# Kernel optimization log

Hardware: AMD Instinct MI355X
Metric: run time of the kernel (lower is better)

The kernel has to match this reference:

```python
import jax, jax.numpy as jnp
import numpy as np

DIM = 256
L = 16            # block_size (query rows per leaf block)
H = 8             # num_heads
D = DIM // H      # head_dim = 32
KC = L + 1        # key count: L leaf nodes + 1 block (mean) node, layout '16x17'
B = 2
N = 32768         # multiple of L -> no padding path
NB = N // L       # 2048 blocks
SCALE = D ** -0.5


def setup_inputs() -> dict:
    key = jax.random.key(0)
    ks = jax.random.split(key, 8)
    x = jax.random.normal(ks[0], (B, N, DIM), jnp.float32)
    attn_mask = jax.random.randint(ks[1], (NB, L, KC), 0, 2, dtype=jnp.int32)
    ar = jnp.arange(L)
    attn_mask = attn_mask.at[:, ar, ar].set(1)  # self always visible -> no all-masked rows
    edge_feats = jax.random.normal(ks[2], (NB, L, KC, 4), jnp.float32)
    s = DIM ** -0.5
    Wqkv = jax.random.normal(ks[3], (3 * DIM, DIM), jnp.float32) * s
    bqkv = jnp.zeros((3 * DIM,), jnp.float32)
    Wproj = jax.random.normal(ks[4], (DIM, DIM), jnp.float32) * s
    bproj = jnp.zeros((DIM,), jnp.float32)
    Wgate = jax.random.normal(ks[5], (H, 4), jnp.float32) * 0.01  # nn.init.normal_(std=0.01)
    bgate = jnp.zeros((H,), jnp.float32)
    return {"x": x, "attn_mask": attn_mask, "edge_feats": edge_feats,
            "Wqkv": Wqkv, "bqkv": bqkv, "Wproj": Wproj, "bproj": bproj,
            "Wgate": Wgate, "bgate": bgate}


def reference(x, attn_mask, edge_feats, Wqkv, bqkv, Wproj, bproj, Wgate, bgate):
    # x: [B, N, C] -> blocks [B, NB, L, C]
    x_blk = x.reshape(B, NB, L, DIM)
    block_node = x_blk.mean(axis=2, keepdims=True)           # virtual block node
    kv = jnp.concatenate([x_blk, block_node], axis=2)         # [B, NB, KC, C]

    # qkv projections (slice of the fused Linear; rows are independent so math is identical)
    q = x_blk @ Wqkv[:DIM].T + bqkv[:DIM]
    k = kv @ Wqkv[DIM:2 * DIM].T + bqkv[DIM:2 * DIM]
    v = kv @ Wqkv[2 * DIM:].T + bqkv[2 * DIM:]
    q = q.reshape(B, NB, L, H, D)
    k = k.reshape(B, NB, KC, H, D)
    v = v.reshape(B, NB, KC, H, D)

    scores = jnp.einsum('bnqhd,bnkhd->bnqkh', q, k) * SCALE   # [B, NB, L, KC, H]

    # physics bias: zero out + set channel 3 = 1 for block node column and self (diagonal)
    ar = jnp.arange(L)
    unit = jnp.array([0.0, 0.0, 0.0, 1.0], edge_feats.dtype)
    bias = edge_feats.at[:, :, L, :].set(unit)                # block-node column
    bias = bias.at[:, ar, ar, :].set(unit)                    # self bias on diagonal
    bias = jnp.broadcast_to(bias[None], (B, NB, L, KC, 4))    # expand over batch

    scores = scores + bias[..., 3:4]

    mask0 = (attn_mask[None] == 0)[..., None]                 # [1, NB, L, KC, 1]
    scores = jnp.where(mask0, -jnp.inf, scores)
    attn = jax.nn.softmax(scores, axis=3)

    gate = jnp.einsum('bnqkf,hf->bnqkh', bias, Wgate) + bgate  # edge-conditioned gate
    gate = jnp.where(mask0, 0.0, gate)

    combined = attn + gate
    out = jnp.einsum('bnqkh,bnkhd->bnqhd', combined, v).reshape(B, N, DIM)
    return out @ Wproj.T + bproj
```

## Files before the change

### kernel.cpp

```cpp
#include <hip/hip_runtime.h>
#include <cstdint>
#include <cstddef>

#define B_SZ 2
#define N_SEQ 32768
#define NB 2048
#define HD 32
#define LQ 16
#define KCNT 17
#define M_ROWS 65536
#define SCALE_F 0.17677669529663687f

typedef __attribute__((ext_vector_type(8))) short sv8;
typedef __attribute__((ext_vector_type(4))) short sv4;
typedef __attribute__((ext_vector_type(4))) float f4;

__device__ __forceinline__ short f2bf(float f) {
  unsigned u = __builtin_bit_cast(unsigned, f);
  u = (u + 0x7FFFu + ((u >> 16) & 1u)) >> 16;
  return (short)u;
}
__device__ __forceinline__ float bf2f(short s) {
  unsigned u = ((unsigned)(unsigned short)s) << 16;
  return __builtin_bit_cast(float, u);
}
__device__ __forceinline__ void gload16(const void* g, void* l) {
  __builtin_amdgcn_global_load_lds(
      (const __attribute__((address_space(1))) unsigned int*)g,
      (__attribute__((address_space(3))) unsigned int*)l, 16, 0, 0);
}
__device__ __forceinline__ f4 mfma16(sv8 a, sv8 b, f4 c) {
  return __builtin_amdgcn_mfma_f32_16x16x32_bf16(a, b, c, 0, 0, 0);
}

__global__ __launch_bounds__(256) void split256(const float* __restrict__ src,
                                                short* __restrict__ dst, int n4) {
  int i = blockIdx.x * 256 + threadIdx.x;
  if (i >= n4) return;
  float4 v = ((const float4*)src)[i];
  size_t row = (size_t)(i >> 6);
  int c = (i & 63) * 4;
  float fv[4] = {v.x, v.y, v.z, v.w};
  sv4 hi, lo;
#pragma unroll
  for (int j = 0; j < 4; ++j) {
    short h = f2bf(fv[j]);
    hi[j] = h;
    lo[j] = f2bf(fv[j] - bf2f(h));
  }
  *(sv4*)&dst[row * 512 + c] = hi;
  *(sv4*)&dst[row * 512 + 256 + c] = lo;
}

__global__ __launch_bounds__(256) void cast256(const float* __restrict__ src,
                                               short* __restrict__ dst, int n4) {
  int i = blockIdx.x * 256 + threadIdx.x;
  if (i >= n4) return;
  float4 v = ((const float4*)src)[i];
  sv4 h = {f2bf(v.x), f2bf(v.y), f2bf(v.z), f2bf(v.w)};
  *(sv4*)&dst[(size_t)i * 4] = h;
}

__global__ __launch_bounds__(256) void gemm_bf_qkv(
    const short* __restrict__ A1, const short* __restrict__ B2,
    const float* __restrict__ bias, short* __restrict__ Qbf,
    short* __restrict__ Kbf, short* __restrict__ Vbf) {
  __shared__ __align__(16) short Ahs[2][128][32];
  __shared__ __align__(16) short Bhs[2][128][32];
  const int tid = threadIdx.x;
  const int w = tid >> 6, l = tid & 63;
  const int wm = w >> 1, wn = w & 1;
  const int bid = blockIdx.x;
  const int chunk = (6 * 512) >> 3;
  const int lbid = (bid & 7) * chunk + (bid >> 3);
  const int nti = lbid % 6, mti = lbid / 6;
  const int m0 = mti * 128, n0 = nti * 128;
  const int lr = l >> 2;
  const int lc = (l & 3) * 8;
  const int fr = l & 15, kg = (l >> 4) * 8;
  f4 acc[4][4] = {};
#pragma unroll
  for (int i = 0; i < 2; ++i) {
    const int row = w * 32 + i * 16;
    gload16(A1 + (size_t)(m0 + row + lr) * 256 + lc, (void*)&Ahs[0][row][0]);
    gload16(B2 + (size_t)(n0 + row + lr) * 512 + lc, (void*)&Bhs[0][row][0]);
  }
  asm volatile("s_waitcnt vmcnt(0)" ::: "memory");
  __builtin_amdgcn_s_barrier();
  int cur = 0;
  for (int s = 0; s < 8; ++s) {
    if (s < 7) {
      const int sk = (s + 1) * 32;
#pragma unroll
      for (int i = 0; i < 2; ++i) {
        const int row = w * 32 + i * 16;
        gload16(A1 + (size_t)(m0 + row + lr) * 256 + sk + lc,
                (void*)&Ahs[cur ^ 1][row][0]);
        gload16(B2 + (size_t)(n0 + row + lr) * 512 + sk + lc,
                (void*)&Bhs[cur ^ 1][row][0]);
      }
    }
    if (s > 0) {
      if (s < 7) asm volatile("s_waitcnt vmcnt(4)" ::: "memory");
      else asm volatile("s_waitcnt vmcnt(0)" ::: "memory");
      __builtin_amdgcn_s_barrier();
    }
    sv8 fa[4], fb[4];
#pragma unroll
    for (int t = 0; t < 4; ++t) {
      fa[t] = *(const sv8*)&Ahs[cur][wm * 64 + t * 16 + fr][kg];
      fb[t] = *(const sv8*)&Bhs[cur][wn * 64 + t * 16 + fr][kg];
    }
#pragma unroll
    for (int mt = 0; mt < 4; ++mt)
#pragma unroll
      for (int nt = 0; nt < 4; ++nt)
        acc[mt][nt] = mfma16(fa[mt], fb[nt], acc[mt][nt]);
    asm volatile("s_waitcnt lgkmcnt(0)" ::: "memory");
    __builtin_amdgcn_s_barrier();
    cur ^= 1;
  }
  short* dst = (nti < 2) ? Qbf : ((nti < 4) ? Kbf : Vbf);
  const int r0 = (l >> 4) * 4;
#pragma unroll
  for (int mt = 0; mt < 4; ++mt)
#pragma unroll
    for (int nt = 0; nt < 4; ++nt) {
      const int n = n0 + wn * 64 + nt * 16 + fr;
      const float bv = bias[n];
      const int nn = n & 255;
      const size_t mb = (size_t)(m0 + wm * 64 + mt * 16 + r0);
#pragma unroll
      for (int j = 0; j < 4; ++j)
        dst[(mb + j) * 256 + nn] = f2bf(acc[mt][nt][j] + bv);
    }
}

__global__ __launch_bounds__(256) void gemm_proj1(
    const short* __restrict__ A1, const short* __restrict__ B2,
    const float* __restrict__ bias, float* __restrict__ C) {
  __shared__ __align__(16) short Ahs[2][128][32];
  __shared__ __align__(16) short Bhs[2][128][32];
  const int tid = threadIdx.x;
  const int w = tid >> 6, l = tid & 63;
  const int wm = w >> 1, wn = w & 1;
  const int bid = blockIdx.x;
  const int chunk = (2 * 512) >> 3;
  const int lbid = (bid & 7) * chunk + (bid >> 3);
  const int nti = lbid % 2, mti = lbid / 2;
  const int m0 = mti * 128, n0 = nti * 128;
  const int lr = l >> 2;
  const int lc = (l & 3) * 8;
  const int fr = l & 15, kg = (l >> 4) * 8;
  f4 acc[4][4] = {};
#pragma unroll
  for (int i = 0; i < 2; ++i) {
    const int row = w * 32 + i * 16;
    gload16(A1 + (size_t)(m0 + row + lr) * 256 + lc, (void*)&Ahs[0][row][0]);
    gload16(B2 + (size_t)(n0 + row + lr) * 512 + lc, (void*)&Bhs[0][row][0]);
  }
  asm volatile("s_waitcnt vmcnt(0)" ::: "memory");
  __builtin_amdgcn_s_barrier();
  int cur = 0;
  for (int s = 0; s < 8; ++s) {
    if (s < 7) {
      const int sk = (s + 1) * 32;
#pragma unroll
      for (int i = 0; i < 2; ++i) {
        const int row = w * 32 + i * 16;
        gload16(A1 + (size_t)(m0 + row + lr) * 256 + sk + lc,
                (void*)&Ahs[cur ^ 1][row][0]);
        gload16(B2 + (size_t)(n0 + row + lr) * 512 + sk + lc,
                (void*)&Bhs[cur ^ 1][row][0]);
      }
    }
    if (s > 0) {
      if (s < 7) asm volatile("s_waitcnt vmcnt(4)" ::: "memory");
      else asm volatile("s_waitcnt vmcnt(0)" ::: "memory");
      __builtin_amdgcn_s_barrier();
    }
    sv8 fa[4], fb[4];
#pragma unroll
    for (int t = 0; t < 4; ++t) {
      fa[t] = *(const sv8*)&Ahs[cur][wm * 64 + t * 16 + fr][kg];
      fb[t] = *(const sv8*)&Bhs[cur][wn * 64 + t * 16 + fr][kg];
    }
#pragma unroll
    for (int mt = 0; mt < 4; ++mt)
#pragma unroll
      for (int nt = 0; nt < 4; ++nt)
        acc[mt][nt] = mfma16(fa[mt], fb[nt], acc[mt][nt]);
    asm volatile("s_waitcnt lgkmcnt(0)" ::: "memory");
    __builtin_amdgcn_s_barrier();
    cur ^= 1;
  }
  const int r0 = (l >> 4) * 4;
#pragma unroll
  for (int mt = 0; mt < 4; ++mt)
#pragma unroll
    for (int nt = 0; nt < 4; ++nt) {
      const int n = n0 + wn * 64 + nt * 16 + fr;
      const float bv = bias[n];
      const size_t mb = (size_t)(m0 + wm * 64 + mt * 16 + r0);
#pragma unroll
      for (int j = 0; j < 4; ++j) C[(mb + j) * 256 + n] = acc[mt][nt][j] + bv;
    }
}

__global__ __launch_bounds__(256, 4) void attn_v7(
    const short* __restrict__ Qb, const short* __restrict__ Kb,
    const short* __restrict__ Vb, const int* __restrict__ amask,
    const float* __restrict__ efeat, const float* __restrict__ Wgate,
    const float* __restrict__ bgate, short* __restrict__ AO) {
  __shared__ __align__(16) short Kl[16 * 264];
  __shared__ __align__(16) short Vl[32 * 264];
  __shared__ __align__(16) short Ol[16 * 264];
  __shared__ float4 Es[LQ * KCNT];
  __shared__ int Ms[LQ * KCNT];

  const int tid = threadIdx.x, g = blockIdx.x;
  const int b = g >> 11, nb = g & (NB - 1);
  const size_t tok0 = (size_t)(b * N_SEQ + nb * LQ);
  const int w = tid >> 6, l = tid & 63;
  const int ln = l & 15, lg = l >> 4;
  const f4 fzero = {0.f, 0.f, 0.f, 0.f};

  sv8 qf[2];
#pragma unroll
  for (int hh = 0; hh < 2; ++hh) {
    const int h = w * 2 + hh;
    qf[hh] = *(const sv8*)(Qb + (tok0 + ln) * 256 + h * 32 + lg * 8);
  }

#pragma unroll
  for (int i = 0; i < 2; ++i) {
    const int f = tid + i * 256;
    const int t = f >> 5, c8 = (f & 31) * 8;
    *(sv8*)&Kl[t * 264 + c8] = *(const sv8*)(Kb + (tok0 + t) * 256 + c8);
    *(sv8*)&Vl[t * 264 + c8] = *(const sv8*)(Vb + (tok0 + t) * 256 + c8);
  }
  {
    const sv8 z = {};
    for (int z8 = tid; z8 < 528; z8 += 256) *(sv8*)&Vl[4224 + z8 * 8] = z;
  }
  {
    const float4* esrc = (const float4*)(efeat + (size_t)nb * LQ * KCNT * 4);
    const int* msrc = amask + (size_t)nb * LQ * KCNT;
    Es[tid] = esrc[tid];
    Ms[tid] = msrc[tid];
    if (tid < LQ * KCNT - 256) {
      Es[256 + tid] = esrc[256 + tid];
      Ms[256 + tid] = msrc[256 + tid];
    }
  }
  __syncthreads();

  const int q = ln;
#pragma unroll
  for (int hh = 0; hh < 2; ++hh) {
    const int h = w * 2 + hh;
    sv8 ka = *(const sv8*)&Kl[ln * 264 + h * 32 + lg * 8];
    f4 sr = mfma16(ka, qf[hh], fzero);

    const float wg0 = Wgate[h * 4], wg1 = Wgate[h * 4 + 1];
    const float wg2 = Wgate[h * 4 + 2], wg3 = Wgate[h * 4 + 3];
    const float bg = bgate[h];

    float rs = sr[0] + sr[1] + sr[2] + sr[3];
    rs += __shfl_xor(rs, 16);
    rs += __shfl_xor(rs, 32);

    float s_[4], gt_[4];
    int vis_[4];
#pragma unroll
    for (int j = 0; j < 4; ++j) {
      const int kc = lg * 4 + j;
      float e0, e1, e2, e3;
      if (kc == q) { e0 = e1 = e2 = 0.f; e3 = 1.f; }
      else { float4 e = Es[q * KCNT + kc]; e0 = e.x; e1 = e.y; e2 = e.z; e3 = e.w; }
      const int m = Ms[q * KCNT + kc];
      vis_[j] = m;
      s_[j] = sr[j] * SCALE_F + e3;
      gt_[j] = m ? (e0 * wg0 + e1 * wg1 + e2 * wg2 + e3 * wg3 + bg) : 0.f;
    }
    const int m16 = Ms[q * KCNT + 16];
    const float s16 = rs * 0.0625f * SCALE_F + 1.0f;

    float mx = -1e30f;
#pragma unroll
    for (int j = 0; j < 4; ++j)
      if (vis_[j]) mx = fmaxf(mx, s_[j]);
    mx = fmaxf(mx, __shfl_xor(mx, 16));
    mx = fmaxf(mx, __shfl_xor(mx, 32));
    if (m16) mx = fmaxf(mx, s16);

    float p_[4], den = 0.f;
#pragma unroll
    for (int j = 0; j < 4; ++j) {
      p_[j] = vis_[j] ? __expf(s_[j] - mx) : 0.f;
      den += p_[j];
    }
    den += __shfl_xor(den, 16);
    den += __shfl_xor(den, 32);
    const float p16 = m16 ? __expf(s16 - mx) : 0.f;
    den += p16;
    const float inv = 1.f / den;
    const float gt16 = m16 ? (wg3 + bg) : 0.f;
    const float cb16 = (p16 * inv + gt16) * 0.0625f;
    float pc[4];
#pragma unroll
    for (int j = 0; j < 4; ++j) pc[j] = p_[j] * inv + gt_[j] + cb16;

    sv8 pa;
#pragma unroll
    for (int e = 0; e < 8; ++e) {
      const int kc = lg * 8 + e;
      const int src = ((kc >> 2) << 4) | q;
      const float v0 = __shfl(pc[e & 3], src);
      pa[e] = (kc < 16) ? f2bf(v0) : (short)0;
    }

#pragma unroll
    for (int t = 0; t < 2; ++t) {
      sv8 vb;
#pragma unroll
      for (int e = 0; e < 8; ++e)
        vb[e] = Vl[(lg * 8 + e) * 264 + h * 32 + t * 16 + ln];
      f4 oacc = mfma16(pa, vb, fzero);
#pragma unroll
      for (int j = 0; j < 4; ++j)
        Ol[(lg * 4 + j) * 264 + h * 32 + t * 16 + ln] = f2bf(oacc[j]);
    }
  }
  __syncthreads();

#pragma unroll
  for (int i = 0; i < 2; ++i) {
    const int f = tid + i * 256;
    const int t = f >> 5, c8 = (f & 31) * 8;
    *(sv8*)(AO + (tok0 + t) * 256 + c8) = *(const sv8*)&Ol[t * 264 + c8];
  }
}

extern "C" void kernel_launch(void* const* d_in, const int* in_sizes, int n_in,
                              void* d_out, int out_size, void* d_ws, size_t ws_size,
                              hipStream_t stream) {
  const float* x = (const float*)d_in[0];
  const int* amask = (const int*)d_in[1];
  const float* efeat = (const float*)d_in[2];
  const float* Wqkv = (const float*)d_in[3];
  const float* bqkv = (const float*)d_in[4];
  const float* Wproj = (const float*)d_in[5];
  const float* bproj = (const float*)d_in[6];
  const float* Wgate = (const float*)d_in[7];
  const float* bgate = (const float*)d_in[8];
  float* out = (float*)d_out;

  char* ws = (char*)d_ws;
  const size_t QB_SZ = (size_t)M_ROWS * 256 * 2;
  const size_t W2Q_SZ = (size_t)768 * 512 * 2;
  const size_t W2P_SZ = (size_t)256 * 512 * 2;
  if (ws_size < 5 * QB_SZ + W2Q_SZ + W2P_SZ) return;

  short* X1 = (short*)ws;
  short* Qbf = (short*)(ws + QB_SZ);
  short* Kbf = (short*)(ws + 2 * QB_SZ);
  short* Vbf = (short*)(ws + 3 * QB_SZ);
  short* AOh = (short*)(ws + 4 * QB_SZ);
  short* W2Q = (short*)(ws + 5 * QB_SZ);
  short* W2P = (short*)(ws + 5 * QB_SZ + W2Q_SZ);

  cast256<<<dim3(M_ROWS * 64 / 256), 256, 0, stream>>>(x, X1, M_ROWS * 64);
  split256<<<dim3(768 * 64 / 256), 256, 0, stream>>>(Wqkv, W2Q, 768 * 64);
  split256<<<dim3(256 * 64 / 256), 256, 0, stream>>>(Wproj, W2P, 256 * 64);
  gemm_bf_qkv<<<dim3(6 * 512), 256, 0, stream>>>(X1, W2Q, bqkv, Qbf, Kbf, Vbf);
  attn_v7<<<dim3(B_SZ * NB), 256, 0, stream>>>(Qbf, Kbf, Vbf, amask, efeat,
                                               Wgate, bgate, AOh);
  gemm_proj1<<<dim3(2 * 512), 256, 0, stream>>>(AOh, W2P, bproj, out);
}
```

Before: 131.8 us.

## Merge cast kernels, drop weight hi/lo split, triple-buffer GEMM pipeline

Replaces the three cast/split launches with one combined cast kernel, cutting launch overhead. Weights are now stored as plain bf16 rather than a hi/lo split, but the old GEMMs only read the hi half anyway, so the results stay the same while weight buffers and strides shrink. Both GEMMs move to a shared macro with a three-stage LDS buffer that prefetches two k-steps ahead, with one barrier per step instead of two. The cost is more shared memory per block, which may lower occupancy.

```diff
diff --git a/kernel.cpp b/kernel.cpp
--- a/kernel.cpp
+++ b/kernel.cpp
@@ -33,177 +33,107 @@
   return __builtin_amdgcn_mfma_f32_16x16x32_bf16(a, b, c, 0, 0, 0);
 }
 
-__global__ __launch_bounds__(256) void split256(const float* __restrict__ src,
-                                                short* __restrict__ dst, int n4) {
-  int i = blockIdx.x * 256 + threadIdx.x;
-  if (i >= n4) return;
-  float4 v = ((const float4*)src)[i];
-  size_t row = (size_t)(i >> 6);
-  int c = (i & 63) * 4;
-  float fv[4] = {v.x, v.y, v.z, v.w};
-  sv4 hi, lo;
-#pragma unroll
-  for (int j = 0; j < 4; ++j) {
-    short h = f2bf(fv[j]);
-    hi[j] = h;
-    lo[j] = f2bf(fv[j] - bf2f(h));
-  }
-  *(sv4*)&dst[row * 512 + c] = hi;
-  *(sv4*)&dst[row * 512 + 256 + c] = lo;
-}
-
-__global__ __launch_bounds__(256) void cast256(const float* __restrict__ src,
-                                               short* __restrict__ dst, int n4) {
-  int i = blockIdx.x * 256 + threadIdx.x;
-  if (i >= n4) return;
-  float4 v = ((const float4*)src)[i];
+__global__ __launch_bounds__(256) void cast_all(
+    const float* __restrict__ x, const float* __restrict__ wq,
+    const float* __restrict__ wp, short* __restrict__ X1,
+    short* __restrict__ W1, short* __restrict__ WP1) {
+  const int i = blockIdx.x * 256 + threadIdx.x;
+  const float* src;
+  short* dst;
+  int off;
+  if (i < 4194304) { src = x; dst = X1; off = i; }
+  else if (i < 4194304 + 49152) { src = wq; dst = W1; off = i - 4194304; }
+  else if (i < 4194304 + 49152 + 16384) { src = wp; dst = WP1; off = i - 4194304 - 49152; }
+  else return;
+  float4 v = ((const float4*)src)[off];
   sv4 h = {f2bf(v.x), f2bf(v.y), f2bf(v.z), f2bf(v.w)};
-  *(sv4*)&dst[(size_t)i * 4] = h;
-}
+  *(sv4*)&dst[(size_t)off * 4] = h;
+}
+
+#define GEMM3_CORE(NT)                                                         \
+  __shared__ __align__(16) short Ahs[3][128][32];                              \
+  __shared__ __align__(16) short Bhs[3][128][32];                              \
+  const int tid = threadIdx.x;                                                 \
+  const int w = tid >> 6, l = tid & 63;                                        \
+  const int wm = w >> 1, wn = w & 1;                                           \
+  const int bid = blockIdx.x;                                                  \
+  const int chunk = (NT * 512) >> 3;                                           \
+  const int lbid = (bid & 7) * chunk + (bid >> 3);                             \
+  const int nti = lbid % (NT), mti = lbid / (NT);                              \
+  const int m0 = mti * 128, n0 = nti * 128;                                    \
+  const int lr = l >> 2, lc = (l & 3) * 8;                                     \
+  const int fr = l & 15, kg = (l >> 4) * 8;                                    \
+  f4 acc[4][4] = {};                                                           \
+  _Pragma("unroll") for (int p = 0; p < 2; ++p) {                              \
+    _Pragma("unroll") for (int i = 0; i < 2; ++i) {                            \
+      const int row = w * 32 + i * 16;                                         \
+      gload16(A1 + (size_t)(m0 + row + lr) * 256 + p * 32 + lc,                \
+              (void*)&Ahs[p][row][0]);                                         \
+      gload16(B1 + (size_t)(n0 + row + lr) * 256 + p * 32 + lc,                \
+              (void*)&Bhs[p][row][0]);                                         \
+    }                                                                          \
+  }                                                                            \
+  for (int s = 0; s < 8; ++s) {                                                \
+    if (s < 7) asm volatile("s_waitcnt vmcnt(4) lgkmcnt(0)" ::: "memory");     \
+    else asm volatile("s_waitcnt vmcnt(0) lgkmcnt(0)" ::: "memory");           \
+    __builtin_amdgcn_s_barrier();                                              \
+    if (s + 2 < 8) {                                                           \
+      const int sk = (s + 2) * 32;                                             \
+      const int bsel = (s + 2) % 3;                                            \
+      _Pragma("unroll") for (int i = 0; i < 2; ++i) {                          \
+        const int row = w * 32 + i * 16;                                       \
+        gload16(A1 + (size_t)(m0 + row + lr) * 256 + sk + lc,                  \
+                (void*)&Ahs[bsel][row][0]);                                    \
+        gload16(B1 + (size_t)(n0 + row + lr) * 256 + sk + lc,                  \
+                (void*)&Bhs[bsel][row][0]);                                    \
+      }                                                                        \
+    }                                                                          \
+    const int cb = s % 3;                                                      \
+    sv8 fa[4], fb[4];                                                          \
+    _Pragma("unroll") for (int t = 0; t < 4; ++t) {                            \
+      fa[t] = *(const sv8*)&Ahs[cb][wm * 64 + t * 16 + fr][kg];                \
+      fb[t] = *(const sv8*)&Bhs[cb][wn * 64 + t * 16 + fr][kg];                \
+    }                                                                          \
+    _Pragma("unroll") for (int mt = 0; mt < 4; ++mt)                           \
+      _Pragma("unroll") for (int nt2 = 0; nt2 < 4; ++nt2)                      \
+        acc[mt][nt2] = mfma16(fa[mt], fb[nt2], acc[mt][nt2]);                  \
+  }
 
 __global__ __launch_bounds__(256) void gemm_bf_qkv(
-    const short* __restrict__ A1, const short* __restrict__ B2,
+    const short* __restrict__ A1, const short* __restrict__ B1,
     const float* __restrict__ bias, short* __restrict__ Qbf,
     short* __restrict__ Kbf, short* __restrict__ Vbf) {
-  __shared__ __align__(16) short Ahs[2][128][32];
-  __shared__ __align__(16) short Bhs[2][128][32];
-  const int tid = threadIdx.x;
-  const int w = tid >> 6, l = tid & 63;
-  const int wm = w >> 1, wn = w & 1;
-  const int bid = blockIdx.x;
-  const int chunk = (6 * 512) >> 3;
-  const int lbid = (bid & 7) * chunk + (bid >> 3);
-  const int nti = lbid % 6, mti = lbid / 6;
-  const int m0 = mti * 128, n0 = nti * 128;
-  const int lr = l >> 2;
-  const int lc = (l & 3) * 8;
-  const int fr = l & 15, kg = (l >> 4) * 8;
-  f4 acc[4][4] = {};
-#pragma unroll
-  for (int i = 0; i < 2; ++i) {
-    const int row = w * 32 + i * 16;
-    gload16(A1 + (size_t)(m0 + row + lr) * 256 + lc, (void*)&Ahs[0][row][0]);
-    gload16(B2 + (size_t)(n0 + row + lr) * 512 + lc, (void*)&Bhs[0][row][0]);
-  }
-  asm volatile("s_waitcnt vmcnt(0)" ::: "memory");
-  __builtin_amdgcn_s_barrier();
-  int cur = 0;
-  for (int s = 0; s < 8; ++s) {
-    if (s < 7) {
-      const int sk = (s + 1) * 32;
-#pragma unroll
-      for (int i = 0; i < 2; ++i) {
-        const int row = w * 32 + i * 16;
-        gload16(A1 + (size_t)(m0 + row + lr) * 256 + sk + lc,
-                (void*)&Ahs[cur ^ 1][row][0]);
-        gload16(B2 + (size_t)(n0 + row + lr) * 512 + sk + lc,
-                (void*)&Bhs[cur ^ 1][row][0]);
-      }
-    }
-    if (s > 0) {
-      if (s < 7) asm volatile("s_waitcnt vmcnt(4)" ::: "memory");
-      else asm volatile("s_waitcnt vmcnt(0)" ::: "memory");
-      __builtin_amdgcn_s_barrier();
-    }
-    sv8 fa[4], fb[4];
-#pragma unroll
-    for (int t = 0; t < 4; ++t) {
-      fa[t] = *(const sv8*)&Ahs[cur][wm * 64 + t * 16 + fr][kg];
-      fb[t] = *(const sv8*)&Bhs[cur][wn * 64 + t * 16 + fr][kg];
-    }
-#pragma unroll
-    for (int mt = 0; mt < 4; ++mt)
-#pragma unroll
-      for (int nt = 0; nt < 4; ++nt)
-        acc[mt][nt] = mfma16(fa[mt], fb[nt], acc[mt][nt]);
-    asm volatile("s_waitcnt lgkmcnt(0)" ::: "memory");
-    __builtin_amdgcn_s_barrier();
-    cur ^= 1;
-  }
+  GEMM3_CORE(6)
   short* dst = (nti < 2) ? Qbf : ((nti < 4) ? Kbf : Vbf);
   const int r0 = (l >> 4) * 4;
 #pragma unroll
   for (int mt = 0; mt < 4; ++mt)
 #pragma unroll
-    for (int nt = 0; nt < 4; ++nt) {
-      const int n = n0 + wn * 64 + nt * 16 + fr;
+    for (int nt2 = 0; nt2 < 4; ++nt2) {
+      const int n = n0 + wn * 64 + nt2 * 16 + fr;
       const float bv = bias[n];
       const int nn = n & 255;
       const size_t mb = (size_t)(m0 + wm * 64 + mt * 16 + r0);
 #pragma unroll
       for (int j = 0; j < 4; ++j)
-        dst[(mb + j) * 256 + nn] = f2bf(acc[mt][nt][j] + bv);
+        dst[(mb + j) * 256 + nn] = f2bf(acc[mt][nt2][j] + bv);
     }
 }
 
 __global__ __launch_bounds__(256) void gemm_proj1(
-    const short* __restrict__ A1, const short* __restrict__ B2,
+    const short* __restrict__ A1, const short* __restrict__ B1,
     const float* __restrict__ bias, float* __restrict__ C) {
-  __shared__ __align__(16) short Ahs[2][128][32];
-  __shared__ __align__(16) short Bhs[2][128][32];
-  const int tid = threadIdx.x;
-  const int w = tid >> 6, l = tid & 63;
-  const int wm = w >> 1, wn = w & 1;
-  const int bid = blockIdx.x;
-  const int chunk = (2 * 512) >> 3;
-  const int lbid = (bid & 7) * chunk + (bid >> 3);
-  const int nti = lbid % 2, mti = lbid / 2;
-  const int m0 = mti * 128, n0 = nti * 128;
-  const int lr = l >> 2;
-  const int lc = (l & 3) * 8;
-  const int fr = l & 15, kg = (l >> 4) * 8;
-  f4 acc[4][4] = {};
-#pragma unroll
-  for (int i = 0; i < 2; ++i) {
-    const int row = w * 32 + i * 16;
-    gload16(A1 + (size_t)(m0 + row + lr) * 256 + lc, (void*)&Ahs[0][row][0]);
-    gload16(B2 + (size_t)(n0 + row + lr) * 512 + lc, (void*)&Bhs[0][row][0]);
-  }
-  asm volatile("s_waitcnt vmcnt(0)" ::: "memory");
-  __builtin_amdgcn_s_barrier();
-  int cur = 0;
-  for (int s = 0; s < 8; ++s) {
-    if (s < 7) {
-      const int sk = (s + 1) * 32;
-#pragma unroll
-      for (int i = 0; i < 2; ++i) {
-        const int row = w * 32 + i * 16;
-        gload16(A1 + (size_t)(m0 + row + lr) * 256 + sk + lc,
-                (void*)&Ahs[cur ^ 1][row][0]);
-        gload16(B2 + (size_t)(n0 + row + lr) * 512 + sk + lc,
-                (void*)&Bhs[cur ^ 1][row][0]);
-      }
-    }
-    if (s > 0) {
-      if (s < 7) asm volatile("s_waitcnt vmcnt(4)" ::: "memory");
-      else asm volatile("s_waitcnt vmcnt(0)" ::: "memory");
-      __builtin_amdgcn_s_barrier();
-    }
-    sv8 fa[4], fb[4];
-#pragma unroll
-    for (int t = 0; t < 4; ++t) {
-      fa[t] = *(const sv8*)&Ahs[cur][wm * 64 + t * 16 + fr][kg];
-      fb[t] = *(const sv8*)&Bhs[cur][wn * 64 + t * 16 + fr][kg];
-    }
-#pragma unroll
-    for (int mt = 0; mt < 4; ++mt)
-#pragma unroll
-      for (int nt = 0; nt < 4; ++nt)
-        acc[mt][nt] = mfma16(fa[mt], fb[nt], acc[mt][nt]);
-    asm volatile("s_waitcnt lgkmcnt(0)" ::: "memory");
-    __builtin_amdgcn_s_barrier();
-    cur ^= 1;
-  }
+  GEMM3_CORE(2)
   const int r0 = (l >> 4) * 4;
 #pragma unroll
   for (int mt = 0; mt < 4; ++mt)
 #pragma unroll
-    for (int nt = 0; nt < 4; ++nt) {
-      const int n = n0 + wn * 64 + nt * 16 + fr;
+    for (int nt2 = 0; nt2 < 4; ++nt2) {
+      const int n = n0 + wn * 64 + nt2 * 16 + fr;
       const float bv = bias[n];
       const size_t mb = (size_t)(m0 + wm * 64 + mt * 16 + r0);
 #pragma unroll
-      for (int j = 0; j < 4; ++j) C[(mb + j) * 256 + n] = acc[mt][nt][j] + bv;
+      for (int j = 0; j < 4; ++j) C[(mb + j) * 256 + n] = acc[mt][nt2][j] + bv;
     }
 }
 
@@ -358,23 +288,23 @@
 
   char* ws = (char*)d_ws;
   const size_t QB_SZ = (size_t)M_ROWS * 256 * 2;
-  const size_t W2Q_SZ = (size_t)768 * 512 * 2;
-  const size_t W2P_SZ = (size_t)256 * 512 * 2;
-  if (ws_size < 5 * QB_SZ + W2Q_SZ + W2P_SZ) return;
+  const size_t W1_SZ = (size_t)768 * 256 * 2;
+  const size_t WP1_SZ = (size_t)256 * 256 * 2;
+  if (ws_size < 5 * QB_SZ + W1_SZ + WP1_SZ) return;
 
   short* X1 = (short*)ws;
   short* Qbf = (short*)(ws + QB_SZ);
   short* Kbf = (short*)(ws + 2 * QB_SZ);
   short* Vbf = (short*)(ws + 3 * QB_SZ);
   short* AOh = (short*)(ws + 4 * QB_SZ);
-  short* W2Q = (short*)(ws + 5 * QB_SZ);
-  short* W2P = (short*)(ws + 5 * QB_SZ + W2Q_SZ);
-
-  cast256<<<dim3(M_ROWS * 64 / 256), 256, 0, stream>>>(x, X1, M_ROWS * 64);
-  split256<<<dim3(768 * 64 / 256), 256, 0, stream>>>(Wqkv, W2Q, 768 * 64);
-  split256<<<dim3(256 * 64 / 256), 256, 0, stream>>>(Wproj, W2P, 256 * 64);
-  gemm_bf_qkv<<<dim3(6 * 512), 256, 0, stream>>>(X1, W2Q, bqkv, Qbf, Kbf, Vbf);
+  short* W1 = (short*)(ws + 5 * QB_SZ);
+  short* WP1 = (short*)(ws + 5 * QB_SZ + W1_SZ);
+
+  const int total_f4 = 4194304 + 49152 + 16384;
+  cast_all<<<dim3((total_f4 + 255) / 256), 256, 0, stream>>>(x, Wqkv, Wproj,
+                                                             X1, W1, WP1);
+  gemm_bf_qkv<<<dim3(6 * 512), 256, 0, stream>>>(X1, W1, bqkv, Qbf, Kbf, Vbf);
   attn_v7<<<dim3(B_SZ * NB), 256, 0, stream>>>(Qbf, Kbf, Vbf, amask, efeat,
                                                Wgate, bgate, AOh);
-  gemm_proj1<<<dim3(2 * 512), 256, 0, stream>>>(AOh, W2P, bproj, out);
-}
+  gemm_proj1<<<dim3(2 * 512), 256, 0, stream>>>(AOh, WP1, bproj, out);
+}
```

New measurement: 125.4 us. 1.05x faster.
